# Optimization experiments

Measured on AMD Instinct MI355X. Metric: run time of the kernel, lower is better.

## Reference

```python
import jax, jax.numpy as jnp
import numpy as np

B, C_IM, N_IN, H, W = 4, 3, 2, 256, 256
NC, MR, NH, NB = 25, 2, 64, 10  # n_class, m_range, num_hidden, num blocks


def _conv(x, w, pad, dil=1):
    return jax.lax.conv_general_dilated(
        x, w, (1, 1), [(pad, pad), (pad, pad)], rhs_dilation=(dil, dil),
        dimension_numbers=('NCHW', 'OIHW', 'NCHW'))


def _bn(x, g, b, m, v):
    # inference-mode BatchNorm2d, eps=1e-5
    inv = g / jnp.sqrt(v + 1e-5)
    return x * inv[:, None, None] + (b - m * inv)[:, None, None]


def setup_inputs() -> dict:
    key = jax.random.key(0)
    ks = iter(jax.random.split(key, 40))
    rn = lambda s, sc=0.05: jax.random.normal(next(ks), s, jnp.float32) * sc
    ru = lambda s: jax.random.uniform(next(ks), s, jnp.float32)
    return {
        'im_input_f': rn((B, C_IM * N_IN, H, W), 1.0),
        'im_input_b': rn((B, C_IM * N_IN, H, W), 1.0),
        'ones': jnp.ones((B, 1, H, W), jnp.float32),
        'm_kernel': ru((1, NC, 2 * MR + 1, 2 * MR + 1)),
        'bn0_g': ru((C_IM * N_IN,)), 'bn0_b': rn((C_IM * N_IN,)),
        'bn0_m': rn((C_IM * N_IN,)), 'bn0_v': ru((C_IM * N_IN,)),
        'conv0_w': rn((NH, C_IM * N_IN, 3, 3)),
        'blk_bn1_g': ru((NB, NH)), 'blk_bn1_b': rn((NB, NH)),
        'blk_bn1_m': rn((NB, NH)), 'blk_bn1_v': ru((NB, NH)),
        'blk_w11': rn((NB, NH, NH, 3, 3)), 'blk_w12': rn((NB, NH, NH, 3, 3)),
        'blk_bn2_g': ru((NB, NH)), 'blk_bn2_b': rn((NB, NH)),
        'blk_bn2_m': rn((NB, NH)), 'blk_bn2_v': ru((NB, NH)),
        'blk_w2': rn((NB, NH, NH, 3, 3)),
        'bnf_g': ru((NH,)), 'bnf_b': rn((NH,)),
        'bnf_m': rn((NH,)), 'bnf_v': ru((NH,)),
        'convf_w': rn((NC, NH, 3, 3)), 'convf_b': rn((NC,)),
    }


def reference(im_input_f, im_input_b, ones, m_kernel,
              bn0_g, bn0_b, bn0_m, bn0_v, conv0_w,
              blk_bn1_g, blk_bn1_b, blk_bn1_m, blk_bn1_v, blk_w11, blk_w12,
              blk_bn2_g, blk_bn2_b, blk_bn2_m, blk_bn2_v, blk_w2,
              bnf_g, bnf_b, bnf_m, bnf_v, convf_w, convf_b):

    def backbone(x):
        x = _conv(_bn(x, bn0_g, bn0_b, bn0_m, bn0_v), conv0_w, 1)

        def block(h, p):
            g1, b1, m1, v1, w11, w12, g2, b2, m2, v2, w2 = p
            out = jax.nn.relu(_bn(h, g1, b1, m1, v1))
            out = _conv(out, w11, 1) + _conv(out, w12, 2, 2)
            out = _conv(jax.nn.relu(_bn(out, g2, b2, m2, v2)), w2, 1)
            return h + out, None

        x, _ = jax.lax.scan(block, x, (blk_bn1_g, blk_bn1_b, blk_bn1_m,
                                       blk_bn1_v, blk_w11, blk_w12,
                                       blk_bn2_g, blk_bn2_b, blk_bn2_m,
                                       blk_bn2_v, blk_w2))
        return _conv(jax.nn.relu(_bn(x, bnf_g, bnf_b, bnf_m, bnf_v)),
                     convf_w, 1) + convf_b[:, None, None]

    motion_f = backbone(im_input_f)
    motion_b = backbone(im_input_b)
    mask_f = jax.nn.softmax(motion_f, axis=1)  # [B, NC, H, W]
    mask_b = jax.nn.softmax(motion_b, axis=1)

    def seg(mask):  # construct_seg, fully batched
        return _conv(ones * mask, m_kernel, MR)  # [B, 1, H, W]

    def pred_im(im_last, mask):  # construct_image: fold (B, im_channel) into batch
        x = (im_last[:, :, None] * mask[:, None]).reshape(B * C_IM, NC, H, W)
        return _conv(x, m_kernel, MR).reshape(B, C_IM, H, W)

    seg_f = seg(mask_f)
    seg_b = seg(mask_b)
    pred_f = pred_im(im_input_f[:, -C_IM:], mask_f)
    pred_b = pred_im(im_input_b[:, -C_IM:], mask_b)
    attn = (seg_f + 1e-5) / (seg_f + seg_b + 2e-5)
    pred = attn * pred_f + (1 - attn) * pred_b
    return (pred, pred_f, mask_f, attn, pred_b, mask_b, 1 - attn)
```

## Files before the change

kernel.cpp:

```cpp
#include <hip/hip_runtime.h>
#include <stdint.h>

typedef unsigned short u16;
typedef float f4 __attribute__((ext_vector_type(4)));
typedef short s8v __attribute__((ext_vector_type(8)));

static __device__ __forceinline__ float bf2f(u16 u){ return __uint_as_float(((unsigned)u)<<16); }
static __device__ __forceinline__ u16 f2bf(float f){
  unsigned u = __float_as_uint(f);
  unsigned r = u + 0x7fffu + ((u>>16)&1u);
  return (u16)(r>>16);
}

#define WS_H    0ull
#define WS_T    67108864ull
#define WS_WDH  134217728ull
#define WS_WDL  135692288ull
#define WS_W2H  137166848ull
#define WS_W2L  137904128ull
#define WS_W0T  138641408ull
#define WS_WFT  138655232ull
#define WS_PAR  138728960ull

#define S0 0
#define T0 8
#define S1 16
#define T1 656
#define S2 1296
#define T2 1936
#define SF 2576
#define TF 2640
#define MK 2704
#define CB 3332

#define O_PRED   0ull
#define O_PREDF  786432ull
#define O_MASKF  1572864ull
#define O_ATTN   8126464ull
#define O_PREDB  8388608ull
#define O_MASKB  9175040ull
#define O_OMA    15728640ull

__global__ void k_prep(const float* g0,const float* b0,const float* m0,const float* v0,
                       const float* g1,const float* b1,const float* m1,const float* v1,
                       const float* g2,const float* b2,const float* m2,const float* v2,
                       const float* gf,const float* bf_,const float* mf,const float* vf,
                       const float* mk,const float* cb, float* par){
  for (int i = threadIdx.x; i < 640; i += 256){
    if (i < 6){ float s = g0[i]/sqrtf(v0[i]+1e-5f); par[S0+i]=s; par[T0+i]=b0[i]-m0[i]*s; }
    { float s = g1[i]/sqrtf(v1[i]+1e-5f); par[S1+i]=s; par[T1+i]=b1[i]-m1[i]*s; }
    { float s = g2[i]/sqrtf(v2[i]+1e-5f); par[S2+i]=s; par[T2+i]=b2[i]-m2[i]*s; }
    if (i < 64){ float s = gf[i]/sqrtf(vf[i]+1e-5f); par[SF+i]=s; par[TF+i]=bf_[i]-mf[i]*s; }
    if (i < 625) par[MK+i] = mk[i];
    if (i < 25)  par[CB+i] = cb[i];
  }
}

__global__ void k_wx2(const float* wf,const float* w0, float* wft, float* w0t){
  int e = blockIdx.x*256 + threadIdx.x;
  if (e < 3456){
    int o = e & 63, r = e >> 6;
    int tap = r % 9, c = r / 9;
    w0t[e] = w0[(o*6+c)*9 + tap];
  } else if (e < 3456 + 18432){
    int e4 = e - 3456;
    int o = e4 & 31, r = e4 >> 5;
    int tap = r % 9, c = r / 9;
    wft[e4] = (o < 25) ? wf[(o*64+c)*9 + tap] : 0.f;
  }
}

__global__ void k_wxm(const float* w11, const float* w12, const float* w2,
                      u16* wdH, u16* wdL, u16* w2H, u16* w2L){
  int e = blockIdx.x*256 + threadIdx.x;
  if (e < 737280){
    int b = e / 73728, f = e % 73728;
    int j = f & 7, l = (f>>3) & 63, cog = (f>>9) & 3, tf = f >> 11;
    int tap = tf % 18, h = tf / 18;
    int co = cog*16 + (l & 15);
    int ci = h*32 + ((l>>4)&3)*8 + j;
    float w = (tap < 9) ? w11[((b*64+co)*64+ci)*9 + tap]
                        : w12[((b*64+co)*64+ci)*9 + (tap-9)];
    u16 hi = f2bf(w);
    wdH[e] = hi; wdL[e] = f2bf(w - bf2f(hi));
  } else if (e < 1105920){
    int e2 = e - 737280;
    int b = e2 / 36864, f = e2 % 36864;
    int j = f & 7, l = (f>>3) & 63, cog = (f>>9) & 3, tf = f >> 11;
    int tap = tf % 9, h = tf / 9;
    int co = cog*16 + (l & 15);
    int ci = h*32 + ((l>>4)&3)*8 + j;
    float w = w2[((b*64+co)*64+ci)*9 + tap];
    u16 hi = f2bf(w);
    w2H[e2] = hi; w2L[e2] = f2bf(w - bf2f(hi));
  }
}

template<int NT,int TAPSET,int OUTMODE>
__global__ __launch_bounds__(256,2) void k_mconv(
    const float* __restrict__ in, float* __restrict__ outb,
    const u16* __restrict__ wH, const u16* __restrict__ wL,
    const float* __restrict__ sc_, const float* __restrict__ tc_){
  __shared__ __align__(16) u16 ldsH[12*36*32];
  __shared__ __align__(16) u16 ldsL[12*36*32];
  __shared__ float lsc[64], ltc[64];
  const int t = threadIdx.x;
  if (t < 64){ lsc[t] = sc_[t]; ltc[t] = tc_[t]; }
  const int img = blockIdx.z, ox = blockIdx.x*32, oy = blockIdx.y*8;
  const int lane = t & 63, wv = t >> 6;
  const int wc = wv & 1, wp = wv >> 1;
  const int P = lane & 15, lhi = lane >> 4;
  const int pbase = (wp*4*36 + P)*64 + lhi*16;
  f4 acc[2][8];
  #pragma unroll
  for (int c2=0;c2<2;c2++)
    #pragma unroll
    for (int n=0;n<8;n++) acc[c2][n] = f4{0.f,0.f,0.f,0.f};
  const s8v* wH8 = (const s8v*)wH;
  const s8v* wL8 = (const s8v*)wL;

  #pragma unroll 1
  for (int h = 0; h < 2; ++h){
    __syncthreads();
    for (int idx = t; idx < 1728; idx += 256){
      int oct = idx / 432, px = idx % 432;
      int pr = px / 36, pc = px % 36;
      int gy = oy + pr - 2, gx = ox + pc - 2;
      int cb = h*32 + oct*8;
      s8v vh = {0,0,0,0,0,0,0,0}, vl = {0,0,0,0,0,0,0,0};
      if ((unsigned)gy < 256u && (unsigned)gx < 256u){
        const float* ip = in + (((size_t)(img*64 + cb))<<16) + gy*256 + gx;
        #pragma unroll
        for (int k=0;k<8;k++){
          float v = fmaxf(ip[(size_t)k<<16]*lsc[cb+k] + ltc[cb+k], 0.f);
          u16 hi = f2bf(v);
          vh[k] = (short)hi;
          vl[k] = (short)f2bf(v - bf2f(hi));
        }
      }
      int ad = px*64 + oct*16;
      *(s8v*)((char*)ldsH + ad) = vh;
      *(s8v*)((char*)ldsL + ad) = vl;
    }
    __syncthreads();
    #pragma unroll
    for (int tap = 0; tap < NT; ++tap){
      int dy, dx;
      if (TAPSET==0){
        if (tap < 9){ dy = tap/3 - 1; dx = tap%3 - 1; }
        else { int dd = tap-9; dy = 2*(dd/3 - 1); dx = 2*(dd%3 - 1); }
      } else { dy = tap/3 - 1; dx = tap%3 - 1; }
      const int tf = h*NT + tap;
      s8v ah0 = wH8[(size_t)((tf*4 + wc*2 + 0)*64 + lane)];
      s8v al0 = wL8[(size_t)((tf*4 + wc*2 + 0)*64 + lane)];
      s8v ah1 = wH8[(size_t)((tf*4 + wc*2 + 1)*64 + lane)];
      s8v al1 = wL8[(size_t)((tf*4 + wc*2 + 1)*64 + lane)];
      #pragma unroll
      for (int n = 0; n < 8; ++n){
        const int off = (((n>>1) + dy + 2)*36 + (n&1)*16 + dx + 2)*64;
        s8v xh = *(const s8v*)((const char*)ldsH + pbase + off);
        s8v xl = *(const s8v*)((const char*)ldsL + pbase + off);
        acc[0][n] = __builtin_amdgcn_mfma_f32_16x16x32_bf16(ah0, xh, acc[0][n], 0,0,0);
        acc[1][n] = __builtin_amdgcn_mfma_f32_16x16x32_bf16(ah1, xh, acc[1][n], 0,0,0);
        acc[0][n] = __builtin_amdgcn_mfma_f32_16x16x32_bf16(al0, xh, acc[0][n], 0,0,0);
        acc[1][n] = __builtin_amdgcn_mfma_f32_16x16x32_bf16(al1, xh, acc[1][n], 0,0,0);
        acc[0][n] = __builtin_amdgcn_mfma_f32_16x16x32_bf16(ah0, xl, acc[0][n], 0,0,0);
        acc[1][n] = __builtin_amdgcn_mfma_f32_16x16x32_bf16(ah1, xl, acc[1][n], 0,0,0);
      }
    }
  }

  #pragma unroll
  for (int c2=0;c2<2;c2++){
    #pragma unroll
    for (int n=0;n<8;n++){
      int y = oy + wp*4 + (n>>1);
      int x = ox + (n&1)*16 + P;
      #pragma unroll
      for (int j=0;j<4;j++){
        int co = (wc*2 + c2)*16 + lhi*4 + j;
        size_t o = (((size_t)(img*64 + co))<<16) + (size_t)(y*256 + x);
        if (OUTMODE==0) outb[o] = acc[c2][n][j];
        else            outb[o] += acc[c2][n][j];
      }
    }
  }
}

template<int NTAPS,int TAPSET,int OUTMODE,int RELU>
__global__ __launch_bounds__(256) void k_conv(
    const float* __restrict__ in, float* __restrict__ outb,
    const float* __restrict__ wt, const float* __restrict__ sc_,
    const float* __restrict__ tc_, int nci){
  __shared__ float lin[4*12*20];
  __shared__ float lw[4*NTAPS*64];
  __shared__ float lsc[64], ltc[64];
  const int t = threadIdx.x;
  const int img = blockIdx.z;
  const int ox = blockIdx.x*16, oy = blockIdx.y*8;
  if (t < 64 && t < nci){ lsc[t] = sc_[t]; ltc[t] = tc_[t]; }
  const int wv = t>>6, lane = t&63;
  const int row = lane>>4, col = lane&15;
  const int co0 = wv*16;
  const int pb0 = (row+2)*20 + col + 2;
  const int pb1 = pb0 + 80;
  f4 a0[4], a1[4];
  #pragma unroll
  for (int q=0;q<4;q++){ a0[q] = f4{0.f,0.f,0.f,0.f}; a1[q] = f4{0.f,0.f,0.f,0.f}; }

  #pragma unroll 1
  for (int c0=0; c0<nci; c0+=4){
    const int cc = (nci - c0 < 4) ? (nci - c0) : 4;
    __syncthreads();
    for (int idx=t; idx<cc*240; idx+=256){
      int c = idx/240, rr = (idx/20)%12, xx = idx%20;
      int gy = oy + rr - 2, gx = ox + xx - 2;
      float v = 0.f;
      if ((unsigned)gy < 256u && (unsigned)gx < 256u){
        v = in[(size_t)(img*nci + c0 + c)*65536 + gy*256 + gx]*lsc[c0+c] + ltc[c0+c];
        if (RELU) v = fmaxf(v, 0.f);
      }
      lin[idx] = v;
    }
    {
      const f4* ws4 = (const f4*)(wt + (size_t)c0*NTAPS*64);
      f4* lw4 = (f4*)lw;
      for (int idx=t; idx<cc*NTAPS*16; idx+=256) lw4[idx] = ws4[idx];
    }
    __syncthreads();
    #pragma unroll 1
    for (int c=0; c<cc; c++){
      const float* lpc = lin + c*240;
      const float* lwc = lw + c*NTAPS*64 + co0;
      #pragma unroll
      for (int tap=0; tap<NTAPS; tap++){
        int dy, dx;
        if (TAPSET==0){
          if (tap < 9){ dy = tap/3 - 1; dx = tap%3 - 1; }
          else      { dy = 2*((tap-9)/3-1); dx = 2*((tap-9)%3-1); }
        } else { dy = tap/3 - 1; dx = tap%3 - 1; }
        float v0 = lpc[pb0 + dy*20 + dx];
        float v1 = lpc[pb1 + dy*20 + dx];
        const f4* wp = (const f4*)(lwc + tap*64);
        #pragma unroll
        for (int q=0;q<4;q++){
          f4 w = wp[q];
          a0[q] += v0*w;
          a1[q] += v1*w;
        }
      }
    }
  }

  size_t p0 = (size_t)((oy+row)*256 + ox + col);
  size_t base = (size_t)(img*64 + co0)*65536;
  if (OUTMODE==0){
    #pragma unroll
    for (int q=0;q<4;q++)
      #pragma unroll
      for (int j=0;j<4;j++){
        outb[base + (size_t)(q*4+j)*65536 + p0]        = a0[q][j];
        outb[base + (size_t)(q*4+j)*65536 + p0 + 1024] = a1[q][j];
      }
  } else {
    #pragma unroll
    for (int q=0;q<4;q++)
      #pragma unroll
      for (int j=0;j<4;j++){
        size_t o0 = base + (size_t)(q*4+j)*65536 + p0;
        outb[o0]        += a0[q][j];
        outb[o0 + 1024] += a1[q][j];
      }
  }
}

__global__ __launch_bounds__(256) void k_fin2(const float* __restrict__ in,
    const float* __restrict__ wft, const float* __restrict__ par,
    float* __restrict__ dmask){
  __shared__ float lin[4*20*20];
  __shared__ float lw[4*9*32];
  __shared__ float lsc[64], ltc[64];
  const int t = threadIdx.x;
  const int img = blockIdx.z;
  const int ox = blockIdx.x*16, oy = blockIdx.y*16;
  if (t < 64){ lsc[t] = par[SF+t]; ltc[t] = par[TF+t]; }
  const int row = t>>4, col = t&15;
  const int pb = (row+2)*20 + col + 2;
  f4 a[8];
  #pragma unroll
  for (int q=0;q<8;q++) a[q] = f4{0.f,0.f,0.f,0.f};

  #pragma unroll 1
  for (int c0=0; c0<64; c0+=4){
    __syncthreads();
    for (int idx=t; idx<4*400; idx+=256){
      int c = idx/400, rr = (idx/20)%20, xx = idx%20;
      int gy = oy + rr - 2, gx = ox + xx - 2;
      float v = 0.f;
      if ((unsigned)gy < 256u && (unsigned)gx < 256u)
        v = fmaxf(in[(size_t)(img*64 + c0 + c)*65536 + gy*256 + gx]*lsc[c0+c] + ltc[c0+c], 0.f);
      lin[idx] = v;
    }
    {
      const f4* ws4 = (const f4*)(wft + (size_t)c0*288);
      f4* lw4 = (f4*)lw;
      for (int idx=t; idx<288; idx+=256) lw4[idx] = ws4[idx];
    }
    __syncthreads();
    #pragma unroll 1
    for (int c=0; c<4; c++){
      const float* lpc = lin + c*400;
      const float* lwc = lw + c*288;
      #pragma unroll
      for (int tap=0; tap<9; tap++){
        int dy = tap/3 - 1, dx = tap%3 - 1;
        float v = lpc[pb + dy*20 + dx];
        const f4* wp = (const f4*)(lwc + tap*32);
        #pragma unroll
        for (int q=0;q<8;q++) a[q] += v*wp[q];
      }
    }
  }

  float lg[25];
  float mx = -3.4e38f;
  #pragma unroll
  for (int o=0;o<25;o++){ lg[o] = a[o>>2][o&3] + par[CB+o]; mx = fmaxf(mx, lg[o]); }
  float s = 0.f;
  #pragma unroll
  for (int o=0;o<25;o++){ lg[o] = expf(lg[o]-mx); s += lg[o]; }
  float inv = 1.f/s;
  size_t p0 = (size_t)((oy+row)*256 + ox + col);
  #pragma unroll
  for (int o=0;o<25;o++)
    dmask[(size_t)(img*25+o)*65536 + p0] = lg[o]*inv;
}

__global__ __launch_bounds__(256) void k_blend(const float* __restrict__ msk,
    const float* __restrict__ imf, const float* __restrict__ imb,
    const float* __restrict__ ones_in, const float* __restrict__ par,
    float* __restrict__ out){
  int pg = blockIdx.x*256 + threadIdx.x;
  int img = pg >> 16, p = pg & 65535;
  int y = p >> 8, x = p & 255;
  float segf = 0.f, segb = 0.f;
  float pf[3] = {0.f,0.f,0.f}, pb[3] = {0.f,0.f,0.f};
  #pragma unroll 1
  for (int u=0; u<5; u++){
    int sy = y - 2 + u;
    if ((unsigned)sy >= 256u) continue;
    #pragma unroll 1
    for (int v=0; v<5; v++){
      int sx = x - 2 + v;
      if ((unsigned)sx >= 256u) continue;
      int sp = sy*256 + sx;
      float sF = 0.f, sB = 0.f;
      #pragma unroll 1
      for (int k=0;k<25;k++){
        float mkv = par[MK + k*25 + u*5 + v];
        sF += mkv * msk[O_MASKF + (size_t)(img*25+k)*65536 + sp];
        sB += mkv * msk[O_MASKB + (size_t)(img*25+k)*65536 + sp];
      }
      float one = ones_in[(size_t)img*65536 + sp];
      segf += one*sF; segb += one*sB;
      #pragma unroll
      for (int c=0;c<3;c++){
        pf[c] += imf[(size_t)(img*6+3+c)*65536 + sp] * sF;
        pb[c] += imb[(size_t)(img*6+3+c)*65536 + sp] * sB;
      }
    }
  }
  float attn = (segf + 1e-5f)/(segf + segb + 2e-5f);
  float na = 1.f - attn;
  #pragma unroll
  for (int c=0;c<3;c++){
    size_t off = (size_t)(img*3+c)*65536 + p;
    out[O_PRED  + off] = attn*pf[c] + na*pb[c];
    out[O_PREDF + off] = pf[c];
    out[O_PREDB + off] = pb[c];
  }
  size_t oa = (size_t)img*65536 + p;
  out[O_ATTN + oa] = attn;
  out[O_OMA  + oa] = na;
}

extern "C" void kernel_launch(void* const* d_in, const int* in_sizes, int n_in,
                              void* d_out, int out_size, void* d_ws, size_t ws_size,
                              hipStream_t stream){
  (void)in_sizes; (void)n_in; (void)out_size; (void)ws_size;
  char* ws = (char*)d_ws;
  float* h   = (float*)(ws + WS_H);
  float* tb  = (float*)(ws + WS_T);
  u16*  wdH  = (u16*)(ws + WS_WDH);
  u16*  wdL  = (u16*)(ws + WS_WDL);
  u16*  w2H  = (u16*)(ws + WS_W2H);
  u16*  w2L  = (u16*)(ws + WS_W2L);
  float* w0t = (float*)(ws + WS_W0T);
  float* wft = (float*)(ws + WS_WFT);
  float* par = (float*)(ws + WS_PAR);
  float* out = (float*)d_out;

  k_prep<<<1,256,0,stream>>>((const float*)d_in[4],(const float*)d_in[5],(const float*)d_in[6],(const float*)d_in[7],
                             (const float*)d_in[9],(const float*)d_in[10],(const float*)d_in[11],(const float*)d_in[12],
                             (const float*)d_in[15],(const float*)d_in[16],(const float*)d_in[17],(const float*)d_in[18],
                             (const float*)d_in[20],(const float*)d_in[21],(const float*)d_in[22],(const float*)d_in[23],
                             (const float*)d_in[3],(const float*)d_in[25], par);
  k_wx2<<<86,256,0,stream>>>((const float*)d_in[24],(const float*)d_in[8], wft, w0t);
  k_wxm<<<4320,256,0,stream>>>((const float*)d_in[13],(const float*)d_in[14],(const float*)d_in[19],
                               wdH, wdL, w2H, w2L);

  dim3 g0(16,32,4);
  dim3 gm(8,32,4);
  dim3 gf(16,16,4);
  for (int dir=0; dir<2; dir++){
    const float* im = (const float*)d_in[dir];
    float* dmask = out + (dir ? O_MASKB : O_MASKF);
    k_conv<9,1,0,0><<<g0,256,0,stream>>>(im, h, w0t, par+S0, par+T0, 6);
    for (int b=0;b<10;b++){
      k_mconv<18,0,0><<<gm,256,0,stream>>>(h, tb, wdH + (size_t)b*73728, wdL + (size_t)b*73728,
                                           par + S1 + b*64, par + T1 + b*64);
      k_mconv<9,1,1><<<gm,256,0,stream>>>(tb, h, w2H + (size_t)b*36864, w2L + (size_t)b*36864,
                                          par + S2 + b*64, par + T2 + b*64);
    }
    k_fin2<<<gf,256,0,stream>>>(h, wft, par, dmask);
  }
  k_blend<<<1024,256,0,stream>>>(out, (const float*)d_in[0], (const float*)d_in[1],
                                 (const float*)d_in[2], par, out);
}
```

Before: 4.095 ms.

## Prefetch next channel half into registers during MFMA compute; restructure blend kernel loops

The residual conv kernel now issues global loads for the second 32-channel half into registers before computing the first half, so memory latency overlaps the MFMA work. The LDS write (BN, ReLU, bf16 hi/lo split) is deferred until after compute. The blend kernel is reorganised to map one row per block with a block-index swizzle, precompute tap offsets and validity, and loop over classes outermost with fully unrolled taps. This gives coalesced row access and better ILP. The cost is much higher register pressure (56 prefetch floats, 50 accumulators), which may reduce occupancy.

Result: slower. 7.016 ms (+71.3%).

```diff
diff --git a/kernel.cpp b/kernel.cpp
--- a/kernel.cpp
+++ b/kernel.cpp
@@ -119,30 +119,51 @@
   const s8v* wH8 = (const s8v*)wH;
   const s8v* wL8 = (const s8v*)wL;
 
-  #pragma unroll 1
-  for (int h = 0; h < 2; ++h){
-    __syncthreads();
-    for (int idx = t; idx < 1728; idx += 256){
-      int oct = idx / 432, px = idx % 432;
-      int pr = px / 36, pc = px % 36;
-      int gy = oy + pr - 2, gx = ox + pc - 2;
-      int cb = h*32 + oct*8;
-      s8v vh = {0,0,0,0,0,0,0,0}, vl = {0,0,0,0,0,0,0,0};
-      if ((unsigned)gy < 256u && (unsigned)gx < 256u){
-        const float* ip = in + (((size_t)(img*64 + cb))<<16) + gy*256 + gx;
-        #pragma unroll
-        for (int k=0;k<8;k++){
-          float v = fmaxf(ip[(size_t)k<<16]*lsc[cb+k] + ltc[cb+k], 0.f);
-          u16 hi = f2bf(v);
-          vh[k] = (short)hi;
-          vl[k] = (short)f2bf(v - bf2f(hi));
+  float rv[7][8];
+  unsigned okm;
+
+  auto LOAD = [&](int h){
+    okm = 0u;
+    #pragma unroll
+    for (int i=0;i<7;i++){
+      int idx = t + (i<<8);
+      if (idx < 1728){
+        int oct = idx & 3, px = idx >> 2;
+        int pr = px / 36, pc = px % 36;
+        int gy = oy + pr - 2, gx = ox + pc - 2;
+        if ((unsigned)gy < 256u && (unsigned)gx < 256u){
+          okm |= 1u << i;
+          const float* ip = in + (((size_t)(img*64 + h*32 + oct*8))<<16) + gy*256 + gx;
+          #pragma unroll
+          for (int k=0;k<8;k++) rv[i][k] = ip[(size_t)k<<16];
         }
       }
-      int ad = px*64 + oct*16;
-      *(s8v*)((char*)ldsH + ad) = vh;
-      *(s8v*)((char*)ldsL + ad) = vl;
-    }
-    __syncthreads();
+    }
+  };
+  auto WRITE = [&](int h){
+    #pragma unroll
+    for (int i=0;i<7;i++){
+      int idx = t + (i<<8);
+      if (idx < 1728){
+        int oct = idx & 3, px = idx >> 2;
+        int cb = h*32 + oct*8;
+        s8v vh = {0,0,0,0,0,0,0,0}, vl = {0,0,0,0,0,0,0,0};
+        if (okm & (1u<<i)){
+          #pragma unroll
+          for (int k=0;k<8;k++){
+            float v = fmaxf(rv[i][k]*lsc[cb+k] + ltc[cb+k], 0.f);
+            u16 hi = f2bf(v);
+            vh[k] = (short)hi;
+            vl[k] = (short)f2bf(v - bf2f(hi));
+          }
+        }
+        int ad = px*64 + oct*16;
+        *(s8v*)((char*)ldsH + ad) = vh;
+        *(s8v*)((char*)ldsL + ad) = vl;
+      }
+    }
+  };
+  auto COMPUTE = [&](int h){
     #pragma unroll
     for (int tap = 0; tap < NT; ++tap){
       int dy, dx;
@@ -168,7 +189,18 @@
         acc[1][n] = __builtin_amdgcn_mfma_f32_16x16x32_bf16(ah1, xl, acc[1][n], 0,0,0);
       }
     }
-  }
+  };
+
+  LOAD(0);
+  __syncthreads();
+  WRITE(0);
+  __syncthreads();
+  LOAD(1);
+  COMPUTE(0);
+  __syncthreads();
+  WRITE(1);
+  __syncthreads();
+  COMPUTE(1);
 
   #pragma unroll
   for (int c2=0;c2<2;c2++){
@@ -340,33 +372,46 @@
     const float* __restrict__ imf, const float* __restrict__ imb,
     const float* __restrict__ ones_in, const float* __restrict__ par,
     float* __restrict__ out){
-  int pg = blockIdx.x*256 + threadIdx.x;
-  int img = pg >> 16, p = pg & 65535;
-  int y = p >> 8, x = p & 255;
+  int bid = blockIdx.x;
+  int swz = (bid & 7)*128 + (bid >> 3);
+  int img = swz >> 8, y = swz & 255, x = threadIdx.x;
+  int p = y*256 + x;
+  int aofs[25]; unsigned vm = 0u;
+  #pragma unroll
+  for (int tap=0; tap<25; tap++){
+    int dy = tap/5-2, dx = tap%5-2, yy = y+dy, xx = x+dx;
+    bool okb = ((unsigned)yy < 256u) && ((unsigned)xx < 256u);
+    aofs[tap] = okb ? (yy*256+xx) : 0;
+    vm |= (okb ? 1u : 0u) << tap;
+  }
+  float sff[25], sfb[25];
+  #pragma unroll
+  for (int i=0;i<25;i++){ sff[i]=0.f; sfb[i]=0.f; }
+  #pragma unroll 1
+  for (int k=0;k<25;k++){
+    const float* mF = msk + O_MASKF + ((size_t)(img*25+k)<<16);
+    const float* mB = msk + O_MASKB + ((size_t)(img*25+k)<<16);
+    #pragma unroll
+    for (int tap=0; tap<25; tap++){
+      float mkv = par[MK + k*25 + tap];
+      float vF = (vm >> tap & 1u) ? mF[aofs[tap]] : 0.f;
+      float vB = (vm >> tap & 1u) ? mB[aofs[tap]] : 0.f;
+      sff[tap] += mkv*vF;
+      sfb[tap] += mkv*vB;
+    }
+  }
   float segf = 0.f, segb = 0.f;
   float pf[3] = {0.f,0.f,0.f}, pb[3] = {0.f,0.f,0.f};
-  #pragma unroll 1
-  for (int u=0; u<5; u++){
-    int sy = y - 2 + u;
-    if ((unsigned)sy >= 256u) continue;
-    #pragma unroll 1
-    for (int v=0; v<5; v++){
-      int sx = x - 2 + v;
-      if ((unsigned)sx >= 256u) continue;
-      int sp = sy*256 + sx;
-      float sF = 0.f, sB = 0.f;
-      #pragma unroll 1
-      for (int k=0;k<25;k++){
-        float mkv = par[MK + k*25 + u*5 + v];
-        sF += mkv * msk[O_MASKF + (size_t)(img*25+k)*65536 + sp];
-        sB += mkv * msk[O_MASKB + (size_t)(img*25+k)*65536 + sp];
-      }
-      float one = ones_in[(size_t)img*65536 + sp];
-      segf += one*sF; segb += one*sB;
+  size_t ib = ((size_t)(img*6))<<16;
+  #pragma unroll
+  for (int tap=0; tap<25; tap++){
+    if (vm >> tap & 1u){
+      float one = ones_in[((size_t)img<<16) + (size_t)aofs[tap]];
+      segf += one*sff[tap]; segb += one*sfb[tap];
       #pragma unroll
       for (int c=0;c<3;c++){
-        pf[c] += imf[(size_t)(img*6+3+c)*65536 + sp] * sF;
-        pb[c] += imb[(size_t)(img*6+3+c)*65536 + sp] * sB;
+        pf[c] += imf[ib + ((size_t)(3+c)<<16) + (size_t)aofs[tap]] * sff[tap];
+        pb[c] += imb[ib + ((size_t)(3+c)<<16) + (size_t)aofs[tap]] * sfb[tap];
       }
     }
   }
@@ -379,7 +424,7 @@
     out[O_PREDF + off] = pf[c];
     out[O_PREDB + off] = pb[c];
   }
-  size_t oa = (size_t)img*65536 + p;
+  size_t oa = ((size_t)img<<16) + (size_t)p;
   out[O_ATTN + oa] = attn;
   out[O_OMA  + oa] = na;
 }
```
